# Kernel tuning notes

Measured on AMD Instinct MI355X. Metric: run time of the kernel, lower is better.

Reference implementation:

```python
import math
import jax, jax.numpy as jnp
import numpy as np

N_HEADS = 16
N_KV_HEADS = 4
HEAD_DIM = 64
DIM = 1024
WINDOW = 16
EPS = 0.01


def _alibi_slopes(n_heads):
    closest = 2 ** math.floor(math.log2(n_heads))
    base = 2.0 ** (-2.0 ** (-(math.log2(closest) - 3)))
    slopes = base ** np.arange(1, closest + 1, dtype=np.float32)
    if closest < n_heads:
        eb = 2.0 ** (-2.0 ** (-(math.log2(2 * closest) - 3)))
        extra = eb ** np.arange(1, 2 * (n_heads - closest) + 1, 2, dtype=np.float32)
        slopes = np.concatenate([slopes, extra])
    return jnp.asarray(slopes[:n_heads])


def _rmsnorm(x, w):
    xf = x.astype(jnp.float32)
    norm = jax.lax.rsqrt(jnp.mean(xf * xf, axis=-1, keepdims=True) + EPS)
    return (xf * norm).astype(x.dtype) * w


def setup_inputs() -> dict:
    key = jax.random.key(0)
    ks = jax.random.split(key, 6)
    B, L = 2, 2048
    s = 1.0 / math.sqrt(DIM)
    return {
        "x": jax.random.normal(ks[0], (B, L, DIM), jnp.float32),
        "wq": jax.random.normal(ks[1], (N_HEADS * HEAD_DIM, DIM), jnp.float32) * s,
        "wk": jax.random.normal(ks[2], (N_KV_HEADS * HEAD_DIM, DIM), jnp.float32) * s,
        "wv": jax.random.normal(ks[3], (N_KV_HEADS * HEAD_DIM, DIM), jnp.float32) * s,
        "wo": jax.random.normal(ks[4], (DIM, N_HEADS * HEAD_DIM), jnp.float32) * s,
        "q_norm_w": jnp.ones((HEAD_DIM,), jnp.float32),
        "k_norm_w": jnp.ones((HEAD_DIM,), jnp.float32),
    }


def reference(x, wq, wk, wv, wo, q_norm_w, k_norm_w):
    B, L, _ = x.shape
    n_rep = N_HEADS // N_KV_HEADS
    q = (x @ wq.T).reshape(B, L, N_HEADS, HEAD_DIM)
    k = (x @ wk.T).reshape(B, L, N_KV_HEADS, HEAD_DIM)
    v = (x @ wv.T).reshape(B, L, N_KV_HEADS, HEAD_DIM)
    q = _rmsnorm(q, q_norm_w)
    k = _rmsnorm(k, k_norm_w)
    # GQA repeat: head h maps to kv head (h % n_kv_heads), matching torch expand order
    k = jnp.broadcast_to(k[:, :, None], (B, L, n_rep, N_KV_HEADS, HEAD_DIM)).reshape(B, L, N_HEADS, HEAD_DIM)
    v = jnp.broadcast_to(v[:, :, None], (B, L, n_rep, N_KV_HEADS, HEAD_DIM)).reshape(B, L, N_HEADS, HEAD_DIM)
    # ALiBi bias with causal + sliding-window mask
    pos = jnp.arange(L)
    rel = pos[None, :] - pos[:, None]  # [L, L], j - i
    slopes = _alibi_slopes(N_HEADS)  # [H]
    bias = slopes[:, None, None] * rel[None].astype(jnp.float32)  # [H, L, L]
    masked = (rel > 0) | (rel < -WINDOW)
    bias = jnp.where(masked[None], -jnp.inf, bias)
    scale = 1.0 / math.sqrt(HEAD_DIM)
    attn = jnp.einsum("bqhd,bkhd->bhqk", q, k) * scale + bias[None]
    attn = jax.nn.softmax(attn, axis=-1)
    out = jnp.einsum("bhqk,bkhd->bqhd", attn, v).reshape(B, L, N_HEADS * HEAD_DIM)
    return out @ wo.T
```

## Files before the change

### kernel.cpp

```cpp
#include <hip/hip_runtime.h>
#include <math.h>

#define DIM 1024
#define NH 16
#define NKV 4
#define HD 64
#define WINDOW 16
#define EPS 0.01f

typedef __bf16 bf16_t;
typedef bf16_t bf16x8 __attribute__((ext_vector_type(8)));
typedef bf16_t bf16x4 __attribute__((ext_vector_type(4)));
typedef float f32x4 __attribute__((ext_vector_type(4)));

__global__ __launch_bounds__(256) void f2bf_all(const float* __restrict__ x,
                                                const float* __restrict__ wq,
                                                const float* __restrict__ wk,
                                                const float* __restrict__ wv,
                                                const float* __restrict__ wo,
                                                bf16_t* __restrict__ xb,
                                                bf16_t* __restrict__ wqkvb,
                                                bf16_t* __restrict__ wob) {
  int i = blockIdx.x * blockDim.x + threadIdx.x;
  const float* src;
  bf16_t* dst;
  int off;
  if (i < 1048576) { src = x; dst = xb; off = i; }
  else if (i < 1310720) { src = wq; dst = wqkvb; off = i - 1048576; }
  else if (i < 1376256) { src = wk; dst = wqkvb + (size_t)1024 * DIM; off = i - 1310720; }
  else if (i < 1441792) { src = wv; dst = wqkvb + (size_t)1280 * DIM; off = i - 1376256; }
  else { src = wo; dst = wob; off = i - 1441792; }
  float4 f = ((const float4*)src)[off];
  bf16x4 o = {(bf16_t)f.x, (bf16_t)f.y, (bf16_t)f.z, (bf16_t)f.w};
  ((bf16x4*)dst)[off] = o;
}


#define GEMM_STAGE(buf, Ag, Bg)                                                 \
  {                                                                             \
    _Pragma("unroll")                                                           \
    for (int it = 0; it < 4; it++) {                                            \
      int c = it * 256 + t;                                                     \
      int r = c >> 3;                                                           \
      int kc = ((c & 7) - r) & 7;                                               \
      __builtin_amdgcn_global_load_lds(                                         \
          (const __attribute__((address_space(1))) void*)((Ag) + (size_t)r * K + kc * 8), \
          (__attribute__((address_space(3))) void*)(As[buf] + c * 8), 16, 0, 0); \
    }                                                                           \
    _Pragma("unroll")                                                           \
    for (int it = 0; it < 2; it++) {                                            \
      int c = it * 256 + t;                                                     \
      int r = c >> 3;                                                           \
      int kc = ((c & 7) - r) & 7;                                               \
      __builtin_amdgcn_global_load_lds(                                         \
          (const __attribute__((address_space(1))) void*)((Bg) + (size_t)r * K + kc * 8), \
          (__attribute__((address_space(3))) void*)(Bs[buf] + c * 8), 16, 0, 0); \
    }                                                                           \
  }

#define GEMM_DBUF_LOOP(Aptr, Bptr)                                              \
  {                                                                             \
    const bf16_t* Abase = Aptr + (size_t)row0 * K;                              \
    const bf16_t* Bbase = Bptr + (size_t)col0 * K;                              \
    GEMM_STAGE(0, Abase, Bbase)                                                 \
    const int nIter = K >> 6;                                                   \
    for (int ki = 0; ki < nIter; ki++) {                                        \
      __syncthreads();                                                          \
      if (ki + 1 < nIter)                                                       \
        GEMM_STAGE((ki + 1) & 1, Abase + (ki + 1) * 64, Bbase + (ki + 1) * 64)  \
      const bf16_t* Ab = As[ki & 1];                                            \
      const bf16_t* Bb = Bs[ki & 1];                                            \
      bf16x8 af[4], bfr[4];                                                     \
      _Pragma("unroll")                                                         \
      for (int mi = 0; mi < 4; mi++) af[mi] = *(const bf16x8*)(Ab + aoff[mi]);  \
      _Pragma("unroll")                                                         \
      for (int ni = 0; ni < 4; ni++) bfr[ni] = *(const bf16x8*)(Bb + boff[ni]); \
      _Pragma("unroll")                                                         \
      for (int mi = 0; mi < 4; mi++)                                            \
        _Pragma("unroll")                                                       \
        for (int ni = 0; ni < 4; ni++)                                          \
          acc[mi][ni] = __builtin_amdgcn_mfma_f32_16x16x32_bf16(af[mi], bfr[ni], \
                                                                acc[mi][ni], 0, 0, 0); \
    }                                                                           \
  }

#define GEMM_REDUCE()                                                           \
  {                                                                             \
    float* Xs = (float*)smem;                                                   \
    __syncthreads();                                                            \
    if (h0) {                                                                   \
      _Pragma("unroll")                                                         \
      for (int j = 0; j < 2; j++)                                               \
        _Pragma("unroll")                                                       \
        for (int ni = 0; ni < 4; ni++)                                          \
          *(f32x4*)(Xs + (size_t)(wid * 64 + ni * 16 + lcol) * 36 + j * 16 + lquad * 4) = \
              acc[j][ni];                                                       \
    } else {                                                                    \
      _Pragma("unroll")                                                         \
      for (int j = 0; j < 2; j++)                                               \
        _Pragma("unroll")                                                       \
        for (int ni = 0; ni < 4; ni++)                                          \
          *(f32x4*)(Xs + (size_t)(wid * 64 + ni * 16 + lcol) * 36 + j * 16 + lquad * 4) = \
              acc[2 + j][ni];                                                   \
    }                                                                           \
    __syncthreads();                                                            \
    if (h0) {                                                                   \
      _Pragma("unroll")                                                         \
      for (int j = 0; j < 2; j++)                                               \
        _Pragma("unroll")                                                       \
        for (int ni = 0; ni < 4; ni++) {                                        \
          f32x4 p = *(const f32x4*)(Xs + (size_t)((wid ^ 1) * 64 + ni * 16 + lcol) * 36 + \
                                    j * 16 + lquad * 4);                        \
          acc[j][ni] = acc[2 + j][ni] + p;                                      \
        }                                                                       \
    } else {                                                                    \
      _Pragma("unroll")                                                         \
      for (int j = 0; j < 2; j++)                                               \
        _Pragma("unroll")                                                       \
        for (int ni = 0; ni < 4; ni++) {                                        \
          f32x4 p = *(const f32x4*)(Xs + (size_t)((wid ^ 1) * 64 + ni * 16 + lcol) * 36 + \
                                    j * 16 + lquad * 4);                        \
          acc[j][ni] = acc[j][ni] + p;                                          \
        }                                                                       \
    }                                                                           \
  }

#define GEMM_PROLOGUE(NBX, BYX)                                                 \
  const int t = threadIdx.x;                                                    \
  const int lane = t & 63;                                                      \
  const int wid = t >> 6;                                                       \
  const int xcd = blockIdx.x & 7;                                               \
  const int jj = blockIdx.x >> 3;                                               \
  const int bx = jj % (NBX);                                                    \
  const int row0 = (xcd * (BYX) + jj / (NBX)) * 128;                            \
  const int col0 = bx * 64;                                                     \
  const int pr = (wid >> 1) * 64;                                               \
  const int h0 = wid & 1;                                                       \
  const int wm = wid * 32;                                                      \
  const int lquad = lane >> 4;                                                  \
  const int lcol = lane & 15;                                                   \
  int aoff[4], boff[4];                                                         \
  _Pragma("unroll")                                                             \
  for (int mi = 0; mi < 4; mi++) {                                              \
    int r = pr + mi * 16 + lcol;                                                \
    aoff[mi] = r * 64 + (((h0 * 4 + lquad) + r) & 7) * 8;                       \
  }                                                                             \
  _Pragma("unroll")                                                             \
  for (int ni = 0; ni < 4; ni++) {                                              \
    int r = ni * 16 + lcol;                                                     \
    boff[ni] = r * 64 + (((h0 * 4 + lquad) + r) & 7) * 8;                       \
  }                                                                             \
  f32x4 acc[4][4] = {};

__global__ __launch_bounds__(256, 3) void gemm_qkv_rms(const bf16_t* __restrict__ A,
                                                       const bf16_t* __restrict__ B,
                                                       bf16_t* __restrict__ C,
                                                       const float* __restrict__ qw,
                                                       const float* __restrict__ kw,
                                                       int M, int N, int K) {
  __shared__ __align__(16) char smem[49152];
  bf16_t (*As)[128 * 64] = (bf16_t(*)[128 * 64])smem;
  bf16_t (*Bs)[64 * 64] = (bf16_t(*)[64 * 64])(smem + 32768);
  GEMM_PROLOGUE(24, 4)
  GEMM_DBUF_LOOP(A, B)
  GEMM_REDUCE()

  const int hcol = bx;
  const bool isv = (hcol >= 20);
  float wreg[4];
  if (!isv) {
    const float* wp = (hcol < 16) ? qw : kw;
#pragma unroll
    for (int ni = 0; ni < 4; ni++) wreg[ni] = wp[ni * 16 + lcol];
  }

#pragma unroll
  for (int mi = 0; mi < 2; mi++) {
#pragma unroll
    for (int r = 0; r < 4; r++) {
      float norm = 1.0f;
      if (!isv) {
        float ss = 0.0f;
#pragma unroll
        for (int ni = 0; ni < 4; ni++) ss += acc[mi][ni][r] * acc[mi][ni][r];
#pragma unroll
        for (int off = 8; off >= 1; off >>= 1) ss += __shfl_xor(ss, off);
        norm = rsqrtf(ss * (1.0f / 64.0f) + EPS);
      }
      size_t base = (size_t)(row0 + wm + mi * 16 + lquad * 4 + r) * N + col0 + lcol;
#pragma unroll
      for (int ni = 0; ni < 4; ni++) {
        float v = acc[mi][ni][r] * norm;
        if (!isv) v *= wreg[ni];
        C[base + ni * 16] = (bf16_t)v;
      }
    }
  }
}

template <typename CT, int NBX, int BYX>
__global__ __launch_bounds__(256, 3) void gemm_bf16(const bf16_t* __restrict__ A,
                                                    const bf16_t* __restrict__ B,
                                                    CT* __restrict__ C,
                                                    int M, int N, int K) {
  __shared__ __align__(16) char smem[49152];
  bf16_t (*As)[128 * 64] = (bf16_t(*)[128 * 64])smem;
  bf16_t (*Bs)[64 * 64] = (bf16_t(*)[64 * 64])(smem + 32768);
  GEMM_PROLOGUE(NBX, BYX)
  GEMM_DBUF_LOOP(A, B)
  GEMM_REDUCE()

#pragma unroll
  for (int mi = 0; mi < 2; mi++)
#pragma unroll
    for (int ni = 0; ni < 4; ni++) {
      size_t base = (size_t)(row0 + wm + mi * 16 + lquad * 4) * N + col0 + ni * 16 + lcol;
#pragma unroll
      for (int r = 0; r < 4; r++)
        C[base + (size_t)r * N] = (CT)acc[mi][ni][r];
    }
}

#define LKP 72
#define LVP 40

__global__ __launch_bounds__(1024) void attn_mfma(const bf16_t* __restrict__ qkv,
                                                  bf16_t* __restrict__ y) {
  __shared__ bf16_t Ks[4][32][LKP];
  __shared__ bf16_t VTs[4][64][LVP];
  __shared__ bf16_t Ps[16][16][LVP];

  const int t = threadIdx.x;
  const int lane = t & 63;
  const int w = t >> 6;
  const int b = blockIdx.x >> 7;
  const int i0loc = (blockIdx.x & 127) << 4;
  const int rowbase = b << 11;
  const int rowg0 = rowbase + i0loc;

  {
    int kvh = t >> 8;
    int key = (t >> 3) & 31;
    int dc = t & 7;
    int jloc = i0loc - 16 + key;
    int rg = rowbase + (jloc < 0 ? 0 : jloc);
    const bf16_t* src = qkv + (size_t)rg * 1536 + 1024 + kvh * 64 + dc * 8;
    bf16x8 kval = *(const bf16x8*)src;
    *(bf16x8*)(&Ks[kvh][key][dc * 8]) = kval;
    bf16x8 vval = *(const bf16x8*)(src + 256);
    int kslot = ((key >> 3) ^ (dc & 3)) * 8 + (key & 7);
#pragma unroll
    for (int e = 0; e < 8; e++) VTs[kvh][dc * 8 + e][kslot] = vval[e];
  }

  const int col = lane & 15;
  const int quad = lane >> 4;
  const int h = w;
  const int kvh = w & 3;
  const float slope = exp2f(-0.5f * (float)(h + 1));

  const bf16_t* qrow = qkv + (size_t)(rowg0 + col) * 1536 + h * 64;
  bf16x8 qf0 = *(const bf16x8*)(qrow + quad * 8);
  bf16x8 qf1 = *(const bf16x8*)(qrow + 32 + quad * 8);

  __syncthreads();

  bf16x8 kf[2][2];
#pragma unroll
  for (int kt = 0; kt < 2; kt++)
#pragma unroll
    for (int kc = 0; kc < 2; kc++)
      kf[kt][kc] = *(const bf16x8*)(&Ks[kvh][kt * 16 + col][kc * 32 + quad * 8]);
  bf16x8 vf[4];
#pragma unroll
  for (int nt = 0; nt < 4; nt++) {
    int dim = nt * 16 + col;
    int kchunk = quad ^ ((dim >> 3) & 3);
    vf[nt] = *(const bf16x8*)(&VTs[kvh][dim][kchunk * 8]);
  }

  f32x4 s0 = {}, s1 = {};
  s0 = __builtin_amdgcn_mfma_f32_16x16x32_bf16(qf0, kf[0][0], s0, 0, 0, 0);
  s0 = __builtin_amdgcn_mfma_f32_16x16x32_bf16(qf1, kf[0][1], s0, 0, 0, 0);
  s1 = __builtin_amdgcn_mfma_f32_16x16x32_bf16(qf0, kf[1][0], s1, 0, 0, 0);
  s1 = __builtin_amdgcn_mfma_f32_16x16x32_bf16(qf1, kf[1][1], s1, 0, 0, 0);

  const bool t0dead = (i0loc == 0);
  float sc0[4], sc1[4];
#pragma unroll
  for (int r = 0; r < 4; r++) {
    int rel0 = col - 16 - (quad * 4 + r);
    int rel1 = rel0 + 16;
    bool m0 = t0dead || (rel0 < -WINDOW);
    bool m1 = (rel1 > 0);
    sc0[r] = m0 ? -INFINITY : s0[r] * 0.125f + slope * (float)rel0;
    sc1[r] = m1 ? -INFINITY : s1[r] * 0.125f + slope * (float)rel1;
  }
  float mx[4], sum[4], p0[4], p1[4];
#pragma unroll
  for (int r = 0; r < 4; r++) mx[r] = fmaxf(sc0[r], sc1[r]);
#pragma unroll
  for (int off = 8; off >= 1; off >>= 1)
#pragma unroll
    for (int r = 0; r < 4; r++) mx[r] = fmaxf(mx[r], __shfl_xor(mx[r], off));
#pragma unroll
  for (int r = 0; r < 4; r++) {
    p0[r] = __expf(sc0[r] - mx[r]);
    p1[r] = __expf(sc1[r] - mx[r]);
    sum[r] = p0[r] + p1[r];
  }
#pragma unroll
  for (int off = 8; off >= 1; off >>= 1)
#pragma unroll
    for (int r = 0; r < 4; r++) sum[r] += __shfl_xor(sum[r], off);

#pragma unroll
  for (int r = 0; r < 4; r++) {
    Ps[w][quad * 4 + r][col] = (bf16_t)p0[r];
    Ps[w][quad * 4 + r][16 + col] = (bf16_t)p1[r];
  }
  bf16x8 pf = *(const bf16x8*)(&Ps[w][col][quad * 8]);

  f32x4 o[4] = {};
#pragma unroll
  for (int nt = 0; nt < 4; nt++)
    o[nt] = __builtin_amdgcn_mfma_f32_16x16x32_bf16(pf, vf[nt], o[nt], 0, 0, 0);

#pragma unroll
  for (int nt = 0; nt < 4; nt++)
#pragma unroll
    for (int r = 0; r < 4; r++)
      y[(size_t)(rowg0 + quad * 4 + r) * 1024 + h * 64 + nt * 16 + col] =
          (bf16_t)(o[nt][r] / sum[r]);
}

extern "C" void kernel_launch(void* const* d_in, const int* in_sizes, int n_in,
                              void* d_out, int out_size, void* d_ws, size_t ws_size,
                              hipStream_t stream) {
  const float* x  = (const float*)d_in[0];
  const float* wq = (const float*)d_in[1];
  const float* wk = (const float*)d_in[2];
  const float* wv = (const float*)d_in[3];
  const float* wo = (const float*)d_in[4];
  const float* qw = (const float*)d_in[5];
  const float* kw = (const float*)d_in[6];
  float* out = (float*)d_out;

  const int M = 4096;

  bf16_t* xb    = (bf16_t*)d_ws;
  bf16_t* wqkvb = xb + (size_t)M * DIM;
  bf16_t* wob   = wqkvb + (size_t)1536 * DIM;
  bf16_t* qkv   = wob + (size_t)DIM * DIM;
  bf16_t* yb    = qkv + (size_t)M * 1536;

  dim3 blk(256);
  f2bf_all<<<1703936 / 256, blk, 0, stream>>>(x, wq, wk, wv, wo, xb, wqkvb, wob);

  gemm_qkv_rms<<<768, blk, 0, stream>>>(xb, wqkvb, qkv, qw, kw, M, 1536, DIM);

  attn_mfma<<<256, dim3(1024), 0, stream>>>(qkv, yb);

  gemm_bf16<float, 16, 4><<<512, blk, 0, stream>>>(yb, wob, out, M, DIM, DIM);
}
```

Before: 123.4 us.

## Split attention into 256-thread blocks with two heads per wave

```diff
diff --git a/kernel.cpp b/kernel.cpp
--- a/kernel.cpp
+++ b/kernel.cpp
@@ -12,6 +12,7 @@
 typedef bf16_t bf16x8 __attribute__((ext_vector_type(8)));
 typedef bf16_t bf16x4 __attribute__((ext_vector_type(4)));
 typedef float f32x4 __attribute__((ext_vector_type(4)));
+
 
 __global__ __launch_bounds__(256) void f2bf_all(const float* __restrict__ x,
                                                 const float* __restrict__ wq,
@@ -224,24 +225,28 @@
 #define LKP 72
 #define LVP 40
 
-__global__ __launch_bounds__(1024) void attn_mfma(const bf16_t* __restrict__ qkv,
-                                                  bf16_t* __restrict__ y) {
+__global__ __launch_bounds__(256) void attn_mfma(const bf16_t* __restrict__ qkv,
+                                                 bf16_t* __restrict__ y) {
   __shared__ bf16_t Ks[4][32][LKP];
   __shared__ bf16_t VTs[4][64][LVP];
-  __shared__ bf16_t Ps[16][16][LVP];
+  __shared__ bf16_t Ps[4][16][LVP];
 
   const int t = threadIdx.x;
   const int lane = t & 63;
-  const int w = t >> 6;
-  const int b = blockIdx.x >> 7;
-  const int i0loc = (blockIdx.x & 127) << 4;
+  const int w4 = t >> 6;
+  const int qt = blockIdx.x >> 1;
+  const int half = blockIdx.x & 1;
+  const int b = qt >> 7;
+  const int i0loc = (qt & 127) << 4;
   const int rowbase = b << 11;
   const int rowg0 = rowbase + i0loc;
 
-  {
-    int kvh = t >> 8;
-    int key = (t >> 3) & 31;
-    int dc = t & 7;
+#pragma unroll
+  for (int it = 0; it < 4; it++) {
+    int cidx = it * 256 + t;
+    int kvh = cidx >> 8;
+    int key = (cidx >> 3) & 31;
+    int dc = cidx & 7;
     int jloc = i0loc - 16 + key;
     int rg = rowbase + (jloc < 0 ? 0 : jloc);
     const bf16_t* src = qkv + (size_t)rg * 1536 + 1024 + kvh * 64 + dc * 8;
@@ -255,13 +260,13 @@
 
   const int col = lane & 15;
   const int quad = lane >> 4;
-  const int h = w;
-  const int kvh = w & 3;
-  const float slope = exp2f(-0.5f * (float)(h + 1));
-
-  const bf16_t* qrow = qkv + (size_t)(rowg0 + col) * 1536 + h * 64;
-  bf16x8 qf0 = *(const bf16x8*)(qrow + quad * 8);
-  bf16x8 qf1 = *(const bf16x8*)(qrow + 32 + quad * 8);
+  const int kvh = w4;
+
+  const bf16_t* qrow0 = qkv + (size_t)(rowg0 + col) * 1536 + (half * 8 + w4) * 64;
+  bf16x8 qfa0 = *(const bf16x8*)(qrow0 + quad * 8);
+  bf16x8 qfa1 = *(const bf16x8*)(qrow0 + 32 + quad * 8);
+  bf16x8 qfb0 = *(const bf16x8*)(qrow0 + 256 + quad * 8);
+  bf16x8 qfb1 = *(const bf16x8*)(qrow0 + 256 + 32 + quad * 8);
 
   __syncthreads();
 
@@ -269,8 +274,8 @@
 #pragma unroll
   for (int kt = 0; kt < 2; kt++)
 #pragma unroll
-    for (int kc = 0; kc < 2; kc++)
-      kf[kt][kc] = *(const bf16x8*)(&Ks[kvh][kt * 16 + col][kc * 32 + quad * 8]);
+    for (int kc2 = 0; kc2 < 2; kc2++)
+      kf[kt][kc2] = *(const bf16x8*)(&Ks[kvh][kt * 16 + col][kc2 * 32 + quad * 8]);
   bf16x8 vf[4];
 #pragma unroll
   for (int nt = 0; nt < 4; nt++) {
@@ -279,59 +284,71 @@
     vf[nt] = *(const bf16x8*)(&VTs[kvh][dim][kchunk * 8]);
   }
 
-  f32x4 s0 = {}, s1 = {};
-  s0 = __builtin_amdgcn_mfma_f32_16x16x32_bf16(qf0, kf[0][0], s0, 0, 0, 0);
-  s0 = __builtin_amdgcn_mfma_f32_16x16x32_bf16(qf1, kf[0][1], s0, 0, 0, 0);
-  s1 = __builtin_amdgcn_mfma_f32_16x16x32_bf16(qf0, kf[1][0], s1, 0, 0, 0);
-  s1 = __builtin_amdgcn_mfma_f32_16x16x32_bf16(qf1, kf[1][1], s1, 0, 0, 0);
-
   const bool t0dead = (i0loc == 0);
-  float sc0[4], sc1[4];
-#pragma unroll
-  for (int r = 0; r < 4; r++) {
-    int rel0 = col - 16 - (quad * 4 + r);
-    int rel1 = rel0 + 16;
-    bool m0 = t0dead || (rel0 < -WINDOW);
-    bool m1 = (rel1 > 0);
-    sc0[r] = m0 ? -INFINITY : s0[r] * 0.125f + slope * (float)rel0;
-    sc1[r] = m1 ? -INFINITY : s1[r] * 0.125f + slope * (float)rel1;
-  }
-  float mx[4], sum[4], p0[4], p1[4];
-#pragma unroll
-  for (int r = 0; r < 4; r++) mx[r] = fmaxf(sc0[r], sc1[r]);
-#pragma unroll
-  for (int off = 8; off >= 1; off >>= 1)
-#pragma unroll
-    for (int r = 0; r < 4; r++) mx[r] = fmaxf(mx[r], __shfl_xor(mx[r], off));
-#pragma unroll
-  for (int r = 0; r < 4; r++) {
-    p0[r] = __expf(sc0[r] - mx[r]);
-    p1[r] = __expf(sc1[r] - mx[r]);
-    sum[r] = p0[r] + p1[r];
-  }
-#pragma unroll
-  for (int off = 8; off >= 1; off >>= 1)
-#pragma unroll
-    for (int r = 0; r < 4; r++) sum[r] += __shfl_xor(sum[r], off);
-
-#pragma unroll
-  for (int r = 0; r < 4; r++) {
-    Ps[w][quad * 4 + r][col] = (bf16_t)p0[r];
-    Ps[w][quad * 4 + r][16 + col] = (bf16_t)p1[r];
-  }
-  bf16x8 pf = *(const bf16x8*)(&Ps[w][col][quad * 8]);
-
-  f32x4 o[4] = {};
-#pragma unroll
-  for (int nt = 0; nt < 4; nt++)
-    o[nt] = __builtin_amdgcn_mfma_f32_16x16x32_bf16(pf, vf[nt], o[nt], 0, 0, 0);
-
-#pragma unroll
-  for (int nt = 0; nt < 4; nt++)
-#pragma unroll
-    for (int r = 0; r < 4; r++)
-      y[(size_t)(rowg0 + quad * 4 + r) * 1024 + h * 64 + nt * 16 + col] =
-          (bf16_t)(o[nt][r] / sum[r]);
+
+#pragma unroll
+  for (int hp = 0; hp < 2; hp++) {
+    const int h = half * 8 + w4 + hp * 4;
+    const float slope = exp2f(-0.5f * (float)(h + 1));
+    bf16x8 qf0 = hp ? qfb0 : qfa0;
+    bf16x8 qf1 = hp ? qfb1 : qfa1;
+
+    f32x4 s0 = {}, s1 = {};
+    s0 = __builtin_amdgcn_mfma_f32_16x16x32_bf16(qf0, kf[0][0], s0, 0, 0, 0);
+    s0 = __builtin_amdgcn_mfma_f32_16x16x32_bf16(qf1, kf[0][1], s0, 0, 0, 0);
+    s1 = __builtin_amdgcn_mfma_f32_16x16x32_bf16(qf0, kf[1][0], s1, 0, 0, 0);
+    s1 = __builtin_amdgcn_mfma_f32_16x16x32_bf16(qf1, kf[1][1], s1, 0, 0, 0);
+
+    float sc0[4], sc1[4];
+#pragma unroll
+    for (int r = 0; r < 4; r++) {
+      int rel0 = col - 16 - (quad * 4 + r);
+      int rel1 = rel0 + 16;
+      bool m0 = t0dead || (rel0 < -WINDOW);
+      bool m1 = (rel1 > 0);
+      sc0[r] = m0 ? -INFINITY : s0[r] * 0.125f + slope * (float)rel0;
+      sc1[r] = m1 ? -INFINITY : s1[r] * 0.125f + slope * (float)rel1;
+    }
+    float mx[4], sum[4], p0[4], p1[4];
+#pragma unroll
+    for (int r = 0; r < 4; r++) mx[r] = fmaxf(sc0[r], sc1[r]);
+#pragma unroll
+    for (int off = 8; off >= 1; off >>= 1)
+#pragma unroll
+      for (int r = 0; r < 4; r++) mx[r] = fmaxf(mx[r], __shfl_xor(mx[r], off));
+#pragma unroll
+    for (int r = 0; r < 4; r++) {
+      p0[r] = __expf(sc0[r] - mx[r]);
+      p1[r] = __expf(sc1[r] - mx[r]);
+      sum[r] = p0[r] + p1[r];
+    }
+#pragma unroll
+    for (int off = 8; off >= 1; off >>= 1)
+#pragma unroll
+      for (int r = 0; r < 4; r++) sum[r] += __shfl_xor(sum[r], off);
+
+#pragma unroll
+    for (int r = 0; r < 4; r++) {
+      Ps[w4][quad * 4 + r][col] = (bf16_t)p0[r];
+      Ps[w4][quad * 4 + r][16 + col] = (bf16_t)p1[r];
+    }
+    bf16x8 pf = *(const bf16x8*)(&Ps[w4][col][quad * 8]);
+
+    f32x4 o[4] = {};
+#pragma unroll
+    for (int nt = 0; nt < 4; nt++)
+      o[nt] = __builtin_amdgcn_mfma_f32_16x16x32_bf16(pf, vf[nt], o[nt], 0, 0, 0);
+
+    float rs[4];
+#pragma unroll
+    for (int r = 0; r < 4; r++) rs[r] = __builtin_amdgcn_rcpf(sum[r]);
+#pragma unroll
+    for (int nt = 0; nt < 4; nt++)
+#pragma unroll
+      for (int r = 0; r < 4; r++)
+        y[(size_t)(rowg0 + quad * 4 + r) * 1024 + h * 64 + nt * 16 + col] =
+            (bf16_t)(o[nt][r] * rs[r]);
+  }
 }
 
 extern "C" void kernel_launch(void* const* d_in, const int* in_sizes, int n_in,
@@ -359,7 +376,7 @@
 
   gemm_qkv_rms<<<768, blk, 0, stream>>>(xb, wqkvb, qkv, qw, kw, M, 1536, DIM);
 
-  attn_mfma<<<256, dim3(1024), 0, stream>>>(qkv, yb);
+  attn_mfma<<<512, blk, 0, stream>>>(qkv, yb);
 
   gemm_bf16<float, 16, 4><<<512, blk, 0, stream>>>(yb, wob, out, M, DIM, DIM);
 }
```

Measured after the change: 124.8 us. Within noise of the previous version (+1.1%).
